# Kernel optimization log

Measured on AMD Instinct MI355X. Metric: run time of the kernel, lower is better.

Reference implementation:

```python
import jax, jax.numpy as jnp
import numpy as np

N, E, G = 20000, 320000, 128
HID, HEADS, LAYERS, IN = 128, 4, 2, 74
EPS = 1e-5


def setup_inputs() -> dict:
    key = jax.random.key(0)
    ks = jax.random.split(key, 10)
    h = jax.random.normal(ks[0], (N, IN), dtype=jnp.float32)
    src = jax.random.randint(ks[1], (E,), 0, N, dtype=jnp.int32)
    dst = jax.random.randint(ks[2], (E,), 0, N, dtype=jnp.int32)
    graph_ids = jnp.sort(jax.random.randint(ks[3], (N,), 0, G, dtype=jnp.int32))
    W0 = jax.random.normal(ks[4], (HEADS, IN, HID), dtype=jnp.float32) / np.sqrt(IN)
    Wr = jax.random.normal(ks[5], (LAYERS - 1, HEADS, HID, HID), dtype=jnp.float32) / np.sqrt(HID)
    att = jax.random.normal(ks[6], (LAYERS, HEADS, 2 * HID), dtype=jnp.float32) / np.sqrt(2 * HID)
    gamma = jnp.ones((LAYERS, HEADS, HID), dtype=jnp.float32)
    beta = jnp.zeros((LAYERS, HEADS, HID), dtype=jnp.float32)
    out_w = jax.random.normal(ks[7], (LAYERS, HID), dtype=jnp.float32) / np.sqrt(HID)
    out_b = jnp.zeros((LAYERS,), dtype=jnp.float32)
    return {"h": h, "src": src, "dst": dst, "graph_ids": graph_ids,
            "W0": W0, "Wr": Wr, "att": att, "gamma": gamma, "beta": beta,
            "out_w": out_w, "out_b": out_b}


def _gat_head(h, W, a, g, b, src, dst):
    # h: [N, F_in], W: [F_in, HID], a: [2*HID]
    z = h @ W                                  # [N, HID]
    zs, zd = z[src], z[dst]                    # [E, HID] gathers
    e = jax.nn.leaky_relu(zs @ a[:HID] + zd @ a[HID:])  # [E] edge logits
    # segment softmax over incoming edges of each dst node
    emax = jax.ops.segment_max(e, dst, num_segments=N)
    ex = jnp.exp(e - emax[dst])
    denom = jax.ops.segment_sum(ex, dst, num_segments=N)
    alpha = ex / denom[dst]
    hout = jax.ops.segment_sum(alpha[:, None] * zs, dst, num_segments=N)  # [N, HID]
    r = jax.nn.relu(hout)
    # BatchNorm1d (training-mode batch stats, biased variance)
    mean = r.mean(0)
    var = r.var(0)
    return g * (r - mean) / jnp.sqrt(var + EPS) + b


def reference(h, src, dst, graph_ids, W0, Wr, att, gamma, beta, out_w, out_b):
    heads = jax.vmap(_gat_head, in_axes=(None, 0, 0, 0, 0, None, None))
    x = h
    for j in range(LAYERS):
        W = W0 if j == 0 else Wr[j - 1]
        hs = heads(x, W, att[j], gamma[j], beta[j], src, dst)  # [HEADS, N, HID]
        hs = jnp.transpose(hs, (1, 0, 2))                       # [N, HEADS, HID]
        score = jax.nn.softmax(hs @ out_w[j] + out_b[j], axis=1)  # [N, HEADS]
        x = jnp.einsum('nh,nhd->nd', score, hs)                 # [N, HID]
    # dgl.mean_nodes: per-graph mean of node features
    counts = jax.ops.segment_sum(jnp.ones((N,), dtype=x.dtype), graph_ids, num_segments=G)
    sums = jax.ops.segment_sum(x, graph_ids, num_segments=G)
    return sums / jnp.maximum(counts, 1.0)[:, None]
```

## Files before the change

kernel.cpp:

```cpp
#include <hip/hip_runtime.h>
#include <hip/hip_bf16.h>

typedef unsigned short u16;
typedef unsigned int u32;
typedef __attribute__((ext_vector_type(8))) short bf16x8;
typedef __attribute__((ext_vector_type(4))) float f32x4;
typedef __attribute__((ext_vector_type(2))) float f32x2;

#define NN 20000
#define NE 320000
#define NG 128
#define HD 128
#define NH 4
#define KIN 74
#define KP0 96
#define BN_EPS 1e-5f
#define SCAN_B 20

__device__ __forceinline__ float bf2f(u16 v){ return __uint_as_float(((u32)v)<<16); }
__device__ __forceinline__ float bflo(u32 v){ return __uint_as_float(v<<16); }
__device__ __forceinline__ float bfhi(u32 v){ return __uint_as_float(v & 0xffff0000u); }
__device__ __forceinline__ u16 f2bf(float f){
    u32 u = __float_as_uint(f);
    return (u16)((u + 0x7fffu + ((u>>16)&1u)) >> 16);
}
__device__ __forceinline__ u32 pack2(float a, float b){
    return (u32)f2bf(a) | ((u32)f2bf(b) << 16);
}

#define PREP_S0 (NN*KP0)
#define PREP_S1 (NH*HD*KP0)
#define PREP_S2 (NH*HD*HD)
#define PREP_TOT (PREP_S0 + PREP_S1 + PREP_S2 + NN + 2048)
__global__ void k_prep(const float* __restrict__ h, const float* __restrict__ W0,
                       const float* __restrict__ Wr, u16* __restrict__ hb,
                       u16* __restrict__ wt0, u16* __restrict__ wt1,
                       int* __restrict__ counts, float* __restrict__ bnstat){
    int i = blockIdx.x*256 + threadIdx.x;
    if(i < PREP_S0){
        int n = i/KP0, k = i - n*KP0;
        hb[i] = (k < KIN) ? f2bf(h[n*KIN + k]) : (u16)0;
        return;
    }
    i -= PREP_S0;
    if(i < PREP_S1){
        int k = i % KP0; int c = (i/KP0) % HD; int hh = i/(KP0*HD);
        wt0[i] = (k < KIN) ? f2bf(W0[(hh*KIN + k)*HD + c]) : (u16)0;
        return;
    }
    i -= PREP_S1;
    if(i < PREP_S2){
        int k = i % HD; int c = (i/HD) % HD; int hh = i/(HD*HD);
        wt1[i] = f2bf(Wr[(hh*HD + k)*HD + c]);
        return;
    }
    i -= PREP_S2;
    if(i < NN){ counts[i] = 0; return; }
    i -= NN;
    if(i < 2048) bnstat[i] = 0.f;
}

__global__ void k_hist(const int* __restrict__ dst, int* __restrict__ counts){
    int e = blockIdx.x*256 + threadIdx.x;
    if(e < NE) atomicAdd(&counts[dst[e]], 1);
}

__global__ void k_scan1(const int* __restrict__ counts, int* __restrict__ rowptr,
                        int* __restrict__ tsum){
    __shared__ int wsum[16];
    int tx = threadIdx.x, lane = tx & 63, wid = tx >> 6;
    int i = blockIdx.x*1024 + tx;
    int v = (i < NN) ? counts[i] : 0;
    int s = v;
    #pragma unroll
    for(int d = 1; d < 64; d <<= 1){ int o = __shfl_up(s, d); if(lane >= d) s += o; }
    if(lane == 63) wsum[wid] = s;
    __syncthreads();
    int woff = 0, total = 0;
    #pragma unroll
    for(int w_ = 0; w_ < 16; ++w_){ int sw = wsum[w_]; total += sw; if(w_ < wid) woff += sw; }
    if(i < NN) rowptr[i] = woff + s - v;
    if(tx == 0) tsum[blockIdx.x] = total;
}

__global__ void k_scan3(int* __restrict__ rowptr, const int* __restrict__ tsum,
                        int* __restrict__ cursor){
    __shared__ int s_off;
    int tx = threadIdx.x;
    if(tx < 64){
        int v = (tx < SCAN_B && tx < (int)blockIdx.x) ? tsum[tx] : 0;
        #pragma unroll
        for(int d = 32; d > 0; d >>= 1) v += __shfl_xor(v, d);
        if(tx == 0) s_off = v;
    }
    __syncthreads();
    int i = blockIdx.x*1024 + tx;
    if(i < NN){
        int val = rowptr[i] + s_off;
        rowptr[i] = val;
        cursor[i] = val;
    }
    if(blockIdx.x == 0 && tx == 0) rowptr[NN] = NE;
}

__global__ void k_scatter(const int* __restrict__ src, const int* __restrict__ dst,
                          int* __restrict__ cursor, int* __restrict__ srcs){
    int e = blockIdx.x*256 + threadIdx.x;
    if(e >= NE) return;
    int d = dst[e];
    int p = atomicAdd(&cursor[d], 1);
    srcs[p] = src[e];
}

template<int KP>
__global__ void k_gemm_mfma(const u16* __restrict__ xb, const u16* __restrict__ wt,
                            u16* __restrict__ z){
    int h = blockIdx.y;
    int tx = threadIdx.x, lane = tx & 63, w = tx >> 6;
    int n0 = blockIdx.x*32 + (w >> 1)*16;
    int c0 = (w & 1)*64;
    int r16 = lane & 15, kg = lane >> 4;
    const u16* ap = xb + (size_t)(n0 + r16)*KP + kg*8;
    const u16* bp = wt + ((size_t)h*HD + c0 + r16)*KP + kg*8;
    f32x4 acc0 = {0.f,0.f,0.f,0.f}, acc1 = {0.f,0.f,0.f,0.f};
    f32x4 acc2 = {0.f,0.f,0.f,0.f}, acc3 = {0.f,0.f,0.f,0.f};
    #pragma unroll
    for(int k0 = 0; k0 < KP; k0 += 32){
        bf16x8 av = *(const bf16x8*)(ap + k0);
        bf16x8 b0 = *(const bf16x8*)(bp + k0);
        bf16x8 b1 = *(const bf16x8*)(bp + 16*KP + k0);
        bf16x8 b2 = *(const bf16x8*)(bp + 32*KP + k0);
        bf16x8 b3 = *(const bf16x8*)(bp + 48*KP + k0);
        acc0 = __builtin_amdgcn_mfma_f32_16x16x32_bf16(av, b0, acc0, 0, 0, 0);
        acc1 = __builtin_amdgcn_mfma_f32_16x16x32_bf16(av, b1, acc1, 0, 0, 0);
        acc2 = __builtin_amdgcn_mfma_f32_16x16x32_bf16(av, b2, acc2, 0, 0, 0);
        acc3 = __builtin_amdgcn_mfma_f32_16x16x32_bf16(av, b3, acc3, 0, 0, 0);
    }
    int nbase = n0 + kg*4;
    u16* zp = z + ((size_t)h*NN + nbase)*HD + c0 + r16;
    #pragma unroll
    for(int reg = 0; reg < 4; ++reg){
        u16* q = zp + (size_t)reg*HD;
        q[0]  = f2bf(acc0[reg]);
        q[16] = f2bf(acc1[reg]);
        q[32] = f2bf(acc2[reg]);
        q[48] = f2bf(acc3[reg]);
    }
}

__global__ void k_dots(const u16* __restrict__ z, const float* __restrict__ attj,
                       float* __restrict__ es, float* __restrict__ ed){
    int tx = threadIdx.x, lane = tx & 63, w = tx >> 6;
    int n = blockIdx.x*4 + w;
    int h = blockIdx.y;
    int ch = lane*2;
    u32 zz = *(const u32*)(z + ((size_t)h*NN + n)*HD + ch);
    float z0 = bflo(zz), z1 = bfhi(zz);
    const float* a = attj + h*2*HD;
    float ps = z0*a[ch]    + z1*a[ch+1];
    float pd = z0*a[HD+ch] + z1*a[HD+ch+1];
    #pragma unroll
    for(int d = 32; d > 0; d >>= 1){ ps += __shfl_xor(ps, d); pd += __shfl_xor(pd, d); }
    if(lane == 0){ es[(size_t)h*NN + n] = ps; ed[(size_t)h*NN + n] = pd; }
}

__global__ void k_aggregate(const int* __restrict__ rowptr, const int* __restrict__ srcs,
                            const float* __restrict__ es, const float* __restrict__ ed,
                            const u16* __restrict__ z, u16* __restrict__ r){
    int tx = threadIdx.x, lane = tx & 63, w = tx >> 6;
    int n = blockIdx.x*4 + w;
    int h = blockIdx.y;
    int p0 = rowptr[n], p1 = rowptr[n+1];
    int eslot = lane >> 4;
    int cidx  = lane & 15;
    const float* esh = es + (size_t)h*NN;
    const u16*   zh  = z  + (size_t)h*NN*HD;
    float edn = ed[(size_t)h*NN + n];
    float ssum = 0.f;
    f32x2 acc[4];
    #pragma unroll
    for(int k = 0; k < 4; ++k) acc[k] = (f32x2){0.f, 0.f};

    for(int base = p0; base < p1; base += 64){
        int p = base + lane;
        int sn = 0; float ex = 0.f;
        if(p < p1){
            sn = srcs[p];
            float e = esh[sn] + edn;
            e = e >= 0.f ? e : 0.01f*e;
            ex = __expf(e);
        }
        ssum += ex;
        int cnt = min(64, p1 - base);
        int niter = (cnt + 7) >> 3;
        for(int i = 0; i < niter; ++i){
            int e0 = i*8 + eslot;
            int e1 = e0 + 4;
            float a0 = __shfl(ex, e0);
            int   s0 = __shfl(sn, e0);
            float a1 = __shfl(ex, e1);
            int   s1 = __shfl(sn, e1);
            uint4 v0 = *(const uint4*)(zh + (size_t)s0*HD + cidx*8);
            uint4 v1 = *(const uint4*)(zh + (size_t)s1*HD + cidx*8);
            f32x2 t;
            t.x = bflo(v0.x); t.y = bfhi(v0.x); acc[0] += a0*t;
            t.x = bflo(v0.y); t.y = bfhi(v0.y); acc[1] += a0*t;
            t.x = bflo(v0.z); t.y = bfhi(v0.z); acc[2] += a0*t;
            t.x = bflo(v0.w); t.y = bfhi(v0.w); acc[3] += a0*t;
            t.x = bflo(v1.x); t.y = bfhi(v1.x); acc[0] += a1*t;
            t.x = bflo(v1.y); t.y = bfhi(v1.y); acc[1] += a1*t;
            t.x = bflo(v1.z); t.y = bfhi(v1.z); acc[2] += a1*t;
            t.x = bflo(v1.w); t.y = bfhi(v1.w); acc[3] += a1*t;
        }
    }
    float c01[8];
    #pragma unroll
    for(int k = 0; k < 4; ++k){
        float a0 = acc[k].x, a1 = acc[k].y;
        a0 += __shfl_xor(a0, 16); a0 += __shfl_xor(a0, 32);
        a1 += __shfl_xor(a1, 16); a1 += __shfl_xor(a1, 32);
        c01[k*2] = a0; c01[k*2+1] = a1;
    }
    #pragma unroll
    for(int d = 32; d > 0; d >>= 1) ssum += __shfl_xor(ssum, d);
    float inv = (ssum > 0.f) ? 1.f/ssum : 0.f;
    if(eslot == 0){
        uint4 o;
        o.x = pack2(fmaxf(c01[0]*inv, 0.f), fmaxf(c01[1]*inv, 0.f));
        o.y = pack2(fmaxf(c01[2]*inv, 0.f), fmaxf(c01[3]*inv, 0.f));
        o.z = pack2(fmaxf(c01[4]*inv, 0.f), fmaxf(c01[5]*inv, 0.f));
        o.w = pack2(fmaxf(c01[6]*inv, 0.f), fmaxf(c01[7]*inv, 0.f));
        *(uint4*)(r + ((size_t)n*NH + h)*HD + cidx*8) = o;
    }
}

__global__ void k_bnreduce(const u16* __restrict__ r, float* __restrict__ bnsum,
                           float* __restrict__ bnsqs){
    int c = blockIdx.x*256 + threadIdx.x;
    int nbeg = blockIdx.y * 160;
    float s = 0.f, s2 = 0.f;
    for(int i = 0; i < 160; ++i){
        float v = bf2f(r[(size_t)(nbeg+i)*512 + c]);
        s += v; s2 += v*v;
    }
    atomicAdd(&bnsum[c], s);
    atomicAdd(&bnsqs[c], s2);
}

__global__ void k_headmix(const u16* __restrict__ r, const float* __restrict__ bnsum,
                          const float* __restrict__ bnsqs, const float* __restrict__ gamma,
                          const float* __restrict__ beta, const float* __restrict__ ow,
                          u16* __restrict__ x){
    __shared__ float sinv[512], sshift[512];
    int tx = threadIdx.x;
    #pragma unroll
    for(int c = tx; c < 512; c += 256){
        float mean = bnsum[c] * (1.f/NN);
        float var  = bnsqs[c] * (1.f/NN) - mean*mean;
        float iv = gamma[c] * rsqrtf(var + BN_EPS);
        sinv[c] = iv;
        sshift[c] = beta[c] - mean*iv;
    }
    __syncthreads();
    int lane = tx & 63, w = tx >> 6;
    int n = blockIdx.x*4 + w;
    int ch = lane*2;
    float rn[NH][2];
    float sc[NH];
    #pragma unroll
    for(int h = 0; h < NH; ++h){
        int c = h*HD + ch;
        u32 zz = *(const u32*)(r + (size_t)n*512 + c);
        float v0 = bflo(zz)*sinv[c]   + sshift[c];
        float v1 = bfhi(zz)*sinv[c+1] + sshift[c+1];
        rn[h][0] = v0; rn[h][1] = v1;
        float p = v0*ow[ch] + v1*ow[ch+1];
        #pragma unroll
        for(int d = 32; d > 0; d >>= 1) p += __shfl_xor(p, d);
        sc[h] = p;
    }
    float m = fmaxf(fmaxf(sc[0], sc[1]), fmaxf(sc[2], sc[3]));
    float e0 = __expf(sc[0]-m), e1 = __expf(sc[1]-m), e2 = __expf(sc[2]-m), e3 = __expf(sc[3]-m);
    float is = 1.f/(e0+e1+e2+e3);
    float x0 = (e0*rn[0][0] + e1*rn[1][0] + e2*rn[2][0] + e3*rn[3][0])*is;
    float x1 = (e0*rn[0][1] + e1*rn[1][1] + e2*rn[2][1] + e3*rn[3][1])*is;
    *(u32*)(x + (size_t)n*HD + ch) = pack2(x0, x1);
}

__global__ void k_gmean(const int* __restrict__ gid, const u16* __restrict__ x,
                        float* __restrict__ out){
    int g = blockIdx.x;
    int tx = threadIdx.x, lane = tx & 63, w = tx >> 6;
    int lo = 0, hi = NN;
    while(lo < hi){ int mid = (lo + hi) >> 1; if(gid[mid] < g) lo = mid + 1; else hi = mid; }
    int start = lo;
    hi = NN;
    while(lo < hi){ int mid = (lo + hi) >> 1; if(gid[mid] < g + 1) lo = mid + 1; else hi = mid; }
    int end = lo;
    float a0 = 0.f, a1 = 0.f;
    for(int n = start + w; n < end; n += 4){
        u32 zz = *(const u32*)(x + (size_t)n*HD + lane*2);
        a0 += bflo(zz);
        a1 += bfhi(zz);
    }
    __shared__ float sm[4][HD];
    sm[w][lane*2]     = a0;
    sm[w][lane*2 + 1] = a1;
    __syncthreads();
    if(tx < HD){
        float s = sm[0][tx] + sm[1][tx] + sm[2][tx] + sm[3][tx];
        float cnt = (float)(end - start);
        out[g*HD + tx] = s / fmaxf(cnt, 1.f);
    }
}

extern "C" void kernel_launch(void* const* d_in, const int* in_sizes, int n_in,
                              void* d_out, int out_size, void* d_ws, size_t ws_size,
                              hipStream_t stream){
    const float* h     = (const float*)d_in[0];
    const int*   src   = (const int*)  d_in[1];
    const int*   dst   = (const int*)  d_in[2];
    const int*   gid   = (const int*)  d_in[3];
    const float* W0    = (const float*)d_in[4];
    const float* Wr    = (const float*)d_in[5];
    const float* att   = (const float*)d_in[6];
    const float* gamma = (const float*)d_in[7];
    const float* beta  = (const float*)d_in[8];
    const float* ow    = (const float*)d_in[9];

    char* p = (char*)d_ws;
    auto alloc = [&](size_t bytes) -> void* {
        void* q = (void*)p;
        p += (bytes + 255) & ~(size_t)255;
        return q;
    };
    u16*   z      = (u16*)  alloc((size_t)NN*NH*HD*2);
    u16*   r      = (u16*)  alloc((size_t)NN*NH*HD*2);
    u16*   x      = (u16*)  alloc((size_t)NN*HD*2);
    u16*   hb     = (u16*)  alloc((size_t)NN*KP0*2);
    u16*   wt0    = (u16*)  alloc((size_t)NH*HD*KP0*2);
    u16*   wt1    = (u16*)  alloc((size_t)NH*HD*HD*2);
    float* es     = (float*)alloc((size_t)NN*NH*4);
    float* ed     = (float*)alloc((size_t)NN*NH*4);
    int*   counts = (int*)  alloc((size_t)NN*4);
    int*   rowptr = (int*)  alloc((size_t)(NN+1)*4);
    int*   cursor = (int*)  alloc((size_t)NN*4);
    int*   srcs   = (int*)  alloc((size_t)NE*4);
    int*   tsum   = (int*)  alloc((size_t)SCAN_B*4);
    float* bnstat = (float*)alloc(2048*4);

    k_prep<<<(PREP_TOT+255)/256, 256, 0, stream>>>(h, W0, Wr, hb, wt0, wt1,
                                                   counts, bnstat);

    k_hist   <<<(NE+255)/256, 256, 0, stream>>>(dst, counts);
    k_scan1  <<<SCAN_B, 1024, 0, stream>>>(counts, rowptr, tsum);
    k_scan3  <<<SCAN_B, 1024, 0, stream>>>(rowptr, tsum, cursor);
    k_scatter<<<(NE+255)/256, 256, 0, stream>>>(src, dst, cursor, srcs);

    for(int j = 0; j < 2; ++j){
        const float* attj = att + j*NH*2*HD;
        if(j == 0) k_gemm_mfma<KP0><<<dim3(NN/32, NH), 256, 0, stream>>>(hb, wt0, z);
        else       k_gemm_mfma<HD> <<<dim3(NN/32, NH), 256, 0, stream>>>(x,  wt1, z);

        k_dots     <<<dim3(NN/4, NH), 256, 0, stream>>>(z, attj, es, ed);
        k_aggregate<<<dim3(NN/4, NH), 256, 0, stream>>>(rowptr, srcs, es, ed, z, r);

        k_bnreduce <<<dim3(2,125), 256, 0, stream>>>(r, bnstat + j*1024, bnstat + j*1024 + 512);
        k_headmix  <<<NN/4, 256, 0, stream>>>(r, bnstat + j*1024, bnstat + j*1024 + 512,
                                              gamma + j*512, beta + j*512, ow + j*HD, x);
    }

    k_gmean<<<NG, 256, 0, stream>>>(gid, x, (float*)d_out);
}
```

Before: 257.9 us.

## Interleave heads in z layout and aggregate all heads per wavefront

Stores z as node-major, head-interleaved ([N,H,HD]) instead of head-major. The aggregate kernel now handles all four heads of a node in one wavefront, with each 16-lane group owning a head, so the gathered rows for a source node are one contiguous 1 KB line. This removes the cross-slot reduction and cuts the grid by four. The cost is less edge-level parallelism per wave, since there are 16 edges per chunk processed serially, and per-lane edge logit loads now go to per-head es arrays.

```diff
diff --git a/kernel.cpp b/kernel.cpp
--- a/kernel.cpp
+++ b/kernel.cpp
@@ -137,10 +137,10 @@
         acc3 = __builtin_amdgcn_mfma_f32_16x16x32_bf16(av, b3, acc3, 0, 0, 0);
     }
     int nbase = n0 + kg*4;
-    u16* zp = z + ((size_t)h*NN + nbase)*HD + c0 + r16;
+    u16* zp = z + ((size_t)nbase*NH + h)*HD + c0 + r16;
     #pragma unroll
     for(int reg = 0; reg < 4; ++reg){
-        u16* q = zp + (size_t)reg*HD;
+        u16* q = zp + (size_t)reg*NH*HD;
         q[0]  = f2bf(acc0[reg]);
         q[16] = f2bf(acc1[reg]);
         q[32] = f2bf(acc2[reg]);
@@ -154,7 +154,7 @@
     int n = blockIdx.x*4 + w;
     int h = blockIdx.y;
     int ch = lane*2;
-    u32 zz = *(const u32*)(z + ((size_t)h*NN + n)*HD + ch);
+    u32 zz = *(const u32*)(z + ((size_t)n*NH + h)*HD + ch);
     float z0 = bflo(zz), z1 = bfhi(zz);
     const float* a = attj + h*2*HD;
     float ps = z0*a[ch]    + z1*a[ch+1];
@@ -169,20 +169,19 @@
                             const u16* __restrict__ z, u16* __restrict__ r){
     int tx = threadIdx.x, lane = tx & 63, w = tx >> 6;
     int n = blockIdx.x*4 + w;
-    int h = blockIdx.y;
+    int h = lane >> 4;
+    int cidx = lane & 15;
     int p0 = rowptr[n], p1 = rowptr[n+1];
-    int eslot = lane >> 4;
-    int cidx  = lane & 15;
     const float* esh = es + (size_t)h*NN;
-    const u16*   zh  = z  + (size_t)h*NN*HD;
     float edn = ed[(size_t)h*NN + n];
+    int bidx = lane & 48;
     float ssum = 0.f;
     f32x2 acc[4];
     #pragma unroll
     for(int k = 0; k < 4; ++k) acc[k] = (f32x2){0.f, 0.f};
 
-    for(int base = p0; base < p1; base += 64){
-        int p = base + lane;
+    for(int base = p0; base < p1; base += 16){
+        int p = base + cidx;
         int sn = 0; float ex = 0.f;
         if(p < p1){
             sn = srcs[p];
@@ -191,17 +190,20 @@
             ex = __expf(e);
         }
         ssum += ex;
-        int cnt = min(64, p1 - base);
-        int niter = (cnt + 7) >> 3;
-        for(int i = 0; i < niter; ++i){
-            int e0 = i*8 + eslot;
-            int e1 = e0 + 4;
-            float a0 = __shfl(ex, e0);
-            int   s0 = __shfl(sn, e0);
-            float a1 = __shfl(ex, e1);
-            int   s1 = __shfl(sn, e1);
-            uint4 v0 = *(const uint4*)(zh + (size_t)s0*HD + cidx*8);
-            uint4 v1 = *(const uint4*)(zh + (size_t)s1*HD + cidx*8);
+        int cnt = min(16, p1 - base);
+        for(int jj = 0; jj < cnt; jj += 4){
+            float a0 = __shfl(ex, bidx + jj);
+            int   s0 = __shfl(sn, bidx + jj);
+            float a1 = __shfl(ex, bidx + jj + 1);
+            int   s1 = __shfl(sn, bidx + jj + 1);
+            float a2 = __shfl(ex, bidx + jj + 2);
+            int   s2 = __shfl(sn, bidx + jj + 2);
+            float a3 = __shfl(ex, bidx + jj + 3);
+            int   s3 = __shfl(sn, bidx + jj + 3);
+            uint4 v0 = *(const uint4*)(z + ((size_t)s0*NH + h)*HD + cidx*8);
+            uint4 v1 = *(const uint4*)(z + ((size_t)s1*NH + h)*HD + cidx*8);
+            uint4 v2 = *(const uint4*)(z + ((size_t)s2*NH + h)*HD + cidx*8);
+            uint4 v3 = *(const uint4*)(z + ((size_t)s3*NH + h)*HD + cidx*8);
             f32x2 t;
             t.x = bflo(v0.x); t.y = bfhi(v0.x); acc[0] += a0*t;
             t.x = bflo(v0.y); t.y = bfhi(v0.y); acc[1] += a0*t;
@@ -211,27 +213,27 @@
             t.x = bflo(v1.y); t.y = bfhi(v1.y); acc[1] += a1*t;
             t.x = bflo(v1.z); t.y = bfhi(v1.z); acc[2] += a1*t;
             t.x = bflo(v1.w); t.y = bfhi(v1.w); acc[3] += a1*t;
+            t.x = bflo(v2.x); t.y = bfhi(v2.x); acc[0] += a2*t;
+            t.x = bflo(v2.y); t.y = bfhi(v2.y); acc[1] += a2*t;
+            t.x = bflo(v2.z); t.y = bfhi(v2.z); acc[2] += a2*t;
+            t.x = bflo(v2.w); t.y = bfhi(v2.w); acc[3] += a2*t;
+            t.x = bflo(v3.x); t.y = bfhi(v3.x); acc[0] += a3*t;
+            t.x = bflo(v3.y); t.y = bfhi(v3.y); acc[1] += a3*t;
+            t.x = bflo(v3.z); t.y = bfhi(v3.z); acc[2] += a3*t;
+            t.x = bflo(v3.w); t.y = bfhi(v3.w); acc[3] += a3*t;
         }
     }
-    float c01[8];
-    #pragma unroll
-    for(int k = 0; k < 4; ++k){
-        float a0 = acc[k].x, a1 = acc[k].y;
-        a0 += __shfl_xor(a0, 16); a0 += __shfl_xor(a0, 32);
-        a1 += __shfl_xor(a1, 16); a1 += __shfl_xor(a1, 32);
-        c01[k*2] = a0; c01[k*2+1] = a1;
-    }
-    #pragma unroll
-    for(int d = 32; d > 0; d >>= 1) ssum += __shfl_xor(ssum, d);
+    ssum += __shfl_xor(ssum, 1);
+    ssum += __shfl_xor(ssum, 2);
+    ssum += __shfl_xor(ssum, 4);
+    ssum += __shfl_xor(ssum, 8);
     float inv = (ssum > 0.f) ? 1.f/ssum : 0.f;
-    if(eslot == 0){
-        uint4 o;
-        o.x = pack2(fmaxf(c01[0]*inv, 0.f), fmaxf(c01[1]*inv, 0.f));
-        o.y = pack2(fmaxf(c01[2]*inv, 0.f), fmaxf(c01[3]*inv, 0.f));
-        o.z = pack2(fmaxf(c01[4]*inv, 0.f), fmaxf(c01[5]*inv, 0.f));
-        o.w = pack2(fmaxf(c01[6]*inv, 0.f), fmaxf(c01[7]*inv, 0.f));
-        *(uint4*)(r + ((size_t)n*NH + h)*HD + cidx*8) = o;
-    }
+    uint4 o;
+    o.x = pack2(fmaxf(acc[0].x*inv, 0.f), fmaxf(acc[0].y*inv, 0.f));
+    o.y = pack2(fmaxf(acc[1].x*inv, 0.f), fmaxf(acc[1].y*inv, 0.f));
+    o.z = pack2(fmaxf(acc[2].x*inv, 0.f), fmaxf(acc[2].y*inv, 0.f));
+    o.w = pack2(fmaxf(acc[3].x*inv, 0.f), fmaxf(acc[3].y*inv, 0.f));
+    *(uint4*)(r + ((size_t)n*NH + h)*HD + cidx*8) = o;
 }
 
 __global__ void k_bnreduce(const u16* __restrict__ r, float* __restrict__ bnsum,
@@ -363,7 +365,7 @@
         else       k_gemm_mfma<HD> <<<dim3(NN/32, NH), 256, 0, stream>>>(x,  wt1, z);
 
         k_dots     <<<dim3(NN/4, NH), 256, 0, stream>>>(z, attj, es, ed);
-        k_aggregate<<<dim3(NN/4, NH), 256, 0, stream>>>(rowptr, srcs, es, ed, z, r);
+        k_aggregate<<<NN/4, 256, 0, stream>>>(rowptr, srcs, es, ed, z, r);
 
         k_bnreduce <<<dim3(2,125), 256, 0, stream>>>(r, bnstat + j*1024, bnstat + j*1024 + 512);
         k_headmix  <<<NN/4, 256, 0, stream>>>(r, bnstat + j*1024, bnstat + j*1024 + 512,
```

Measured after the change: 266.7 us. 3.4% more time.
